# Performance work log

Measured on AMD Instinct MI355X. Metric: run time of the kernel, lower is better.

Reference implementation:

```python
import jax, jax.numpy as jnp
import numpy as np


def setup_inputs() -> dict:
    key = jax.random.key(0)
    ks = jax.random.split(key, 11)
    B, S, D = 2, 2048, 1024
    s = 0.02
    return {
        "query": jax.random.normal(ks[0], (B, S, D), jnp.float32),
        "key": jax.random.normal(ks[1], (B, S, D), jnp.float32),
        "value": jax.random.normal(ks[2], (B, S, D), jnp.float32),
        "Wq": jax.random.normal(ks[3], (D, D), jnp.float32) * s,
        "bq": jnp.zeros((D,), jnp.float32),
        "Wk": jax.random.normal(ks[4], (D, D), jnp.float32) * s,
        "bk": jnp.zeros((D,), jnp.float32),
        "Wv": jax.random.normal(ks[5], (D, D), jnp.float32) * s,
        "bv": jnp.zeros((D,), jnp.float32),
        "Wo": jax.random.normal(ks[6], (D, D), jnp.float32) * s,
        "bo": jnp.zeros((D,), jnp.float32),
        "nheads": 16,
    }


def reference(query, key, value, Wq, bq, Wk, bk, Wv, bv, Wo, bo, nheads):
    B, Sq, D = query.shape
    Sk = key.shape[1]
    hd = D // nheads  # head dim
    q = (query @ Wq.T + bq).reshape(B, Sq, nheads, hd)
    k = (key @ Wk.T + bk).reshape(B, Sk, nheads, hd)
    v = (value @ Wv.T + bv).reshape(B, Sk, nheads, hd)
    score = jnp.einsum("bqhd,bkhd->bhqk", q, k)
    # mask == 'triu': strictly-upper-triangular entries set to -inf (causal)
    causal = jnp.triu(jnp.ones((Sq, Sk), dtype=bool), k=1)
    score = jnp.where(causal, -jnp.inf, score)
    # NOTE: original scales by sqrt(score.shape[-1]) == sqrt(kv_len), not sqrt(head_dim)
    scale = np.float32(1.0 / np.sqrt(Sk))
    att = jax.nn.softmax(score * scale, axis=-1)
    ret = jnp.einsum("bhqk,bkhd->bqhd", att, v).reshape(B, Sq, D)
    out = ret @ Wo.T + bo  # dropout is identity in eval mode
    return (out, att)
```

## Files before the change

### kernel.cpp

```cpp
#include <hip/hip_runtime.h>
#include <cstdint>
#include <cstddef>
#include <type_traits>

typedef __attribute__((ext_vector_type(8))) __bf16 bf16x8;
typedef __attribute__((ext_vector_type(4))) __bf16 bf16x4;
typedef __attribute__((ext_vector_type(4))) float f32x4;
typedef __attribute__((ext_vector_type(4))) unsigned short u16x4;

__device__ __forceinline__ f32x4 mfma16(bf16x8 a, bf16x8 b, f32x4 c) {
  return __builtin_amdgcn_mfma_f32_16x16x32_bf16(a, b, c, 0, 0, 0);
}

__device__ __forceinline__ void load_lds16(const void* g, void* l) {
  auto gp = reinterpret_cast<const __attribute__((address_space(1))) uint32_t*>(
      reinterpret_cast<uintptr_t>(g));
  auto lp = reinterpret_cast<__attribute__((address_space(3))) uint32_t*>(
      static_cast<uint32_t>(reinterpret_cast<uintptr_t>(l)));
  __builtin_amdgcn_global_load_lds(gp, lp, 16, 0, 0);
}

static constexpr float SCALE = 0.022097086912079608f;

static constexpr size_t OFF_XQ = 0;
static constexpr size_t OFF_XK = 4194304;
static constexpr size_t OFF_XV = 8388608;
static constexpr size_t OFF_WQ = 12582912;
static constexpr size_t OFF_WK = 13631488;
static constexpr size_t OFF_WV = 14680064;
static constexpr size_t OFF_WO = 15728640;
static constexpr size_t OFF_QB = 16777216;
static constexpr size_t OFF_KB = 20971520;
static constexpr size_t OFF_VT = 25165824;
static constexpr size_t OFF_RT = 29360128;

__global__ __launch_bounds__(256) void convert_all(
    const float* __restrict__ q, const float* __restrict__ k,
    const float* __restrict__ v, const float* __restrict__ wq,
    const float* __restrict__ wk, const float* __restrict__ wv,
    const float* __restrict__ wo, __bf16* __restrict__ ws)
{
  const int total = 2097152;
  for (int i = blockIdx.x * blockDim.x + threadIdx.x; i < total;
       i += gridDim.x * blockDim.x) {
    const float* src; size_t dstoff; int rel;
    if (i < 1572864) {
      if (i < 524288)       { src = q;  dstoff = OFF_XQ; rel = i; }
      else if (i < 1048576) { src = k;  dstoff = OFF_XK; rel = i - 524288; }
      else                  { src = v;  dstoff = OFF_XV; rel = i - 1048576; }
    } else if (i < 1835008) {
      if (i < 1703936)      { src = wq; dstoff = OFF_WQ; rel = i - 1572864; }
      else                  { src = wk; dstoff = OFF_WK; rel = i - 1703936; }
    } else if (i < 1966080) { src = wv; dstoff = OFF_WV; rel = i - 1835008; }
    else                    { src = wo; dstoff = OFF_WO; rel = i - 1966080; }
    float4 f0 = reinterpret_cast<const float4*>(src)[(size_t)rel * 2];
    float4 f1 = reinterpret_cast<const float4*>(src)[(size_t)rel * 2 + 1];
    bf16x8 o;
    o[0] = (__bf16)f0.x; o[1] = (__bf16)f0.y; o[2] = (__bf16)f0.z; o[3] = (__bf16)f0.w;
    o[4] = (__bf16)f1.x; o[5] = (__bf16)f1.y; o[6] = (__bf16)f1.z; o[7] = (__bf16)f1.w;
    *reinterpret_cast<bf16x8*>(ws + dstoff + (size_t)rel * 8) = o;
  }
}

__device__ __forceinline__ void gemm_body(
    const __bf16* __restrict__ A, const __bf16* __restrict__ Bm,
    const float* __restrict__ bias, void* __restrict__ Cout,
    int M, int N, int K, int mode, int m0, int n0,
    __bf16* As, __bf16* Bs)
{
  const int t = threadIdx.x;
  const int lane = t & 63, r = lane & 15, g = lane >> 4;
  const int w = t >> 6, wm = w >> 1, wn = w & 1;
  const int srow = t >> 3, scol = (t & 7) * 8;

  const f32x4 fzero = {0.f, 0.f, 0.f, 0.f};
  f32x4 acc[4][4];
#pragma unroll
  for (int x = 0; x < 4; x++)
#pragma unroll
    for (int y = 0; y < 4; y++) acc[x][y] = fzero;

  auto stage = [&](int buf, int k0) {
#pragma unroll
    for (int i = 0; i < 4; i++) {
      load_lds16(A  + (size_t)(m0 + i * 32 + srow) * K + k0 + scol, &As[buf * 8192 + i * 2048 + t * 8]);
      load_lds16(Bm + (size_t)(n0 + i * 32 + srow) * K + k0 + scol, &Bs[buf * 8192 + i * 2048 + t * 8]);
    }
  };

  const int NT = K / 64;
  stage(0, 0);
  asm volatile("s_waitcnt vmcnt(0)" ::: "memory");
  __syncthreads();
  int cur = 0;
  for (int kt = 0; kt < NT; ++kt) {
    if (kt + 1 < NT) stage(cur ^ 1, (kt + 1) * 64);
    const __bf16* Ab = &As[cur * 8192];
    const __bf16* Bb = &Bs[cur * 8192];
#pragma unroll
    for (int kk = 0; kk < 2; kk++) {
      bf16x8 af[4], bfv[4];
#pragma unroll
      for (int x = 0; x < 4; x++)
        af[x] = *reinterpret_cast<const bf16x8*>(&Ab[(wm * 64 + x * 16 + r) * 64 + kk * 32 + g * 8]);
#pragma unroll
      for (int y = 0; y < 4; y++)
        bfv[y] = *reinterpret_cast<const bf16x8*>(&Bb[(wn * 64 + y * 16 + r) * 64 + kk * 32 + g * 8]);
#pragma unroll
      for (int x = 0; x < 4; x++)
#pragma unroll
        for (int y = 0; y < 4; y++)
          acc[x][y] = mfma16(af[x], bfv[y], acc[x][y]);
    }
    asm volatile("s_waitcnt vmcnt(0)" ::: "memory");
    __syncthreads();
    cur ^= 1;
  }

#pragma unroll
  for (int x = 0; x < 4; x++)
#pragma unroll
    for (int y = 0; y < 4; y++) {
#pragma unroll
      for (int j = 0; j < 4; j++) {
        int row = m0 + wm * 64 + x * 16 + g * 4 + j;
        int col = n0 + wn * 64 + y * 16 + r;
        float val = acc[x][y][j];
        if (mode == 0 || mode == 1) {
          val += bias[col];
          int b = row >> 11, s = row & 2047, h = col >> 6, d = col & 63;
          ((__bf16*)Cout)[(((size_t)(b * 16 + h) * 2048 + s) << 6) + d] = (__bf16)val;
        } else if (mode == 2) {
          val += bias[row];
          int h = row >> 6, d = row & 63, b = col >> 11, s = col & 2047;
          ((__bf16*)Cout)[(((size_t)(b * 16 + h) * 64 + d) << 11) + s] = (__bf16)val;
        } else {
          val += bias[col];
          __builtin_nontemporal_store(val, &((float*)Cout)[(size_t)row * N + col]);
        }
      }
    }
}

__global__ __launch_bounds__(256) void gemm_qkv(
    __bf16* __restrict__ ws, const float* __restrict__ bq,
    const float* __restrict__ bk, const float* __restrict__ bv)
{
  __shared__ __align__(16) __bf16 As[2 * 8192];
  __shared__ __align__(16) __bf16 Bs[2 * 8192];
  const int z = blockIdx.z;
  if (z == 0) {
    gemm_body(ws + OFF_XQ, ws + OFF_WQ, bq, ws + OFF_QB, 4096, 1024, 1024, 0,
              blockIdx.y * 128, blockIdx.x * 128, As, Bs);
  } else if (z == 1) {
    gemm_body(ws + OFF_XK, ws + OFF_WK, bk, ws + OFF_KB, 4096, 1024, 1024, 1,
              blockIdx.y * 128, blockIdx.x * 128, As, Bs);
  } else {
    gemm_body(ws + OFF_WV, ws + OFF_XV, bv, ws + OFF_VT, 1024, 4096, 1024, 2,
              blockIdx.x * 128, blockIdx.y * 128, As, Bs);
  }
}

__global__ __launch_bounds__(256) void gemm_o(
    const __bf16* __restrict__ Rt, const __bf16* __restrict__ Wo,
    const float* __restrict__ bo, float* __restrict__ out)
{
  __shared__ __align__(16) __bf16 As[2 * 8192];
  __shared__ __align__(16) __bf16 Bs[2 * 8192];
  gemm_body(Rt, Wo, bo, out, 4096, 1024, 1024, 3,
            blockIdx.y * 128, blockIdx.x * 128, As, Bs);
}

__global__ __launch_bounds__(256) void attn_kernel(
    const __bf16* __restrict__ Qb, const __bf16* __restrict__ Kb,
    const __bf16* __restrict__ Vt, __bf16* __restrict__ Rt,
    float* __restrict__ att)
{
  __shared__ __align__(16) __bf16 Ks[128 * 68];
  __shared__ __align__(16) __bf16 Vts[64 * 132];
  __shared__ __align__(16) __bf16 Ps[128 * 132];

  const int t = threadIdx.x;
  const int lane = t & 63, r = lane & 15, g = lane >> 4;
  const int w = t >> 6;
  const int p = blockIdx.x;
  const int workid = (p & 7) * 64 + (p >> 3);
  const int bh = workid >> 4;
  const int xx = workid & 15;
  const int qb = ((bh >> 1) & 1) ? 15 - xx : xx;
  const int q0 = qb * 128;
  const __bf16* Qg = Qb + (size_t)bh * 2048 * 64;
  const __bf16* Kg = Kb + (size_t)bh * 2048 * 64;
  const __bf16* Vg = Vt + (size_t)bh * 64 * 2048;
  float* attb = att + (size_t)bh * 2048 * 2048 + (size_t)q0 * 2048;

  const int lrow = t >> 3, lcol = (t & 7) * 8;
  const int vrow = t >> 4, vcol = (t & 15) * 8;

  const f32x4 fzero = {0.f, 0.f, 0.f, 0.f};

  bf16x8 aq[2][2];
#pragma unroll
  for (int mf = 0; mf < 2; mf++)
#pragma unroll
    for (int kk = 0; kk < 2; kk++)
      aq[mf][kk] = *reinterpret_cast<const bf16x8*>(
          Qg + (size_t)(q0 + w * 32 + mf * 16 + r) * 64 + kk * 32 + g * 8);

  auto compute_scores = [&](f32x4(&accs)[2][8]) {
#pragma unroll
    for (int mf = 0; mf < 2; mf++)
#pragma unroll
      for (int nf = 0; nf < 8; nf++) accs[mf][nf] = fzero;
    __builtin_amdgcn_s_setprio(1);
#pragma unroll
    for (int kk = 0; kk < 2; kk++) {
#pragma unroll
      for (int nf = 0; nf < 8; nf++) {
        bf16x8 bk = *reinterpret_cast<const bf16x8*>(&Ks[(nf * 16 + r) * 68 + kk * 32 + g * 8]);
        accs[0][nf] = mfma16(aq[0][kk], bk, accs[0][nf]);
        accs[1][nf] = mfma16(aq[1][kk], bk, accs[1][nf]);
      }
    }
    __builtin_amdgcn_s_setprio(0);
  };

  float rs[2][4];
#pragma unroll
  for (int mf = 0; mf < 2; mf++)
#pragma unroll
    for (int j = 0; j < 4; j++) rs[mf][j] = 0.f;

  bf16x8 rk[4];
#pragma unroll
  for (int i = 0; i < 4; i++)
    rk[i] = *reinterpret_cast<const bf16x8*>(Kg + (size_t)(i * 32 + lrow) * 64 + lcol);

  for (int kt = 0; kt <= qb; ++kt) {
    __syncthreads();
#pragma unroll
    for (int i = 0; i < 4; i++)
      *reinterpret_cast<bf16x8*>(&Ks[(i * 32 + lrow) * 68 + lcol]) = rk[i];
    __syncthreads();
    if (kt < qb) {
#pragma unroll
      for (int i = 0; i < 4; i++)
        rk[i] = *reinterpret_cast<const bf16x8*>(Kg + (size_t)((kt + 1) * 128 + i * 32 + lrow) * 64 + lcol);
    }
    f32x4 accs[2][8];
    compute_scores(accs);

    auto p1body = [&](auto maskc) {
      constexpr bool MASK = decltype(maskc)::value;
#pragma unroll
      for (int mf = 0; mf < 2; mf++) {
        float es[4] = {0.f, 0.f, 0.f, 0.f};
#pragma unroll
        for (int nf = 0; nf < 8; nf++) {
          int col = kt * 128 + nf * 16 + r;
#pragma unroll
          for (int j = 0; j < 4; j++) {
            float e = __expf(accs[mf][nf][j] * SCALE);
            if (MASK) {
              int rowg = q0 + w * 32 + mf * 16 + g * 4 + j;
              e = (col <= rowg) ? e : 0.f;
            }
            es[j] += e;
          }
        }
#pragma unroll
        for (int j = 0; j < 4; j++) {
          float v2 = es[j];
          v2 += __shfl_xor(v2, 1, 64);
          v2 += __shfl_xor(v2, 2, 64);
          v2 += __shfl_xor(v2, 4, 64);
          v2 += __shfl_xor(v2, 8, 64);
          rs[mf][j] += v2;
        }
      }
    };
    if (kt == qb) p1body(std::integral_constant<bool, true>{});
    else          p1body(std::integral_constant<bool, false>{});
  }

  float rl[2][4];
#pragma unroll
  for (int mf = 0; mf < 2; mf++)
#pragma unroll
    for (int j = 0; j < 4; j++) rl[mf][j] = 1.0f / rs[mf][j];

  f32x4 accr[2][4];
#pragma unroll
  for (int mf = 0; mf < 2; mf++)
#pragma unroll
    for (int nf = 0; nf < 4; nf++) accr[mf][nf] = fzero;

  bf16x8 rv[4];
#pragma unroll
  for (int i = 0; i < 4; i++) {
    rk[i] = *reinterpret_cast<const bf16x8*>(Kg + (size_t)(i * 32 + lrow) * 64 + lcol);
    rv[i] = *reinterpret_cast<const bf16x8*>(Vg + (size_t)(i * 16 + vrow) * 2048 + vcol);
  }

  for (int kt = 0; kt <= qb; ++kt) {
    __syncthreads();
#pragma unroll
    for (int i = 0; i < 4; i++) {
      *reinterpret_cast<bf16x8*>(&Ks[(i * 32 + lrow) * 68 + lcol]) = rk[i];
      *reinterpret_cast<bf16x8*>(&Vts[(i * 16 + vrow) * 132 + vcol]) = rv[i];
    }
    __syncthreads();
    if (kt < qb) {
#pragma unroll
      for (int i = 0; i < 4; i++) {
        rk[i] = *reinterpret_cast<const bf16x8*>(Kg + (size_t)((kt + 1) * 128 + i * 32 + lrow) * 64 + lcol);
        rv[i] = *reinterpret_cast<const bf16x8*>(Vg + (size_t)(i * 16 + vrow) * 2048 + (kt + 1) * 128 + vcol);
      }
    }
    f32x4 accs[2][8];
    compute_scores(accs);

    auto p2body = [&](auto maskc) {
      constexpr bool MASK = decltype(maskc)::value;
#pragma unroll
      for (int mf = 0; mf < 2; mf++) {
#pragma unroll
        for (int nf = 0; nf < 8; nf++) {
          int col = kt * 128 + nf * 16 + r;
#pragma unroll
          for (int j = 0; j < 4; j++) {
            int rowl = w * 32 + mf * 16 + g * 4 + j;
            float e = __expf(accs[mf][nf][j] * SCALE);
            if (MASK) {
              e = (col <= q0 + rowl) ? e : 0.f;
            }
            float pp = e * rl[mf][j];
            Ps[rowl * 132 + nf * 16 + r] = (__bf16)pp;
          }
        }
      }
    };
    if (kt == qb) p2body(std::integral_constant<bool, true>{});
    else          p2body(std::integral_constant<bool, false>{});

    __syncthreads();
    __builtin_amdgcn_s_setprio(1);
#pragma unroll
    for (int kk2 = 0; kk2 < 4; kk2++) {
      bf16x8 ap0 = *reinterpret_cast<const bf16x8*>(&Ps[(w * 32 + r) * 132 + kk2 * 32 + g * 8]);
      bf16x8 ap1 = *reinterpret_cast<const bf16x8*>(&Ps[(w * 32 + 16 + r) * 132 + kk2 * 32 + g * 8]);
#pragma unroll
      for (int nf2 = 0; nf2 < 4; nf2++) {
        bf16x8 bv_ = *reinterpret_cast<const bf16x8*>(&Vts[(nf2 * 16 + r) * 132 + kk2 * 32 + g * 8]);
        accr[0][nf2] = mfma16(ap0, bv_, accr[0][nf2]);
        accr[1][nf2] = mfma16(ap1, bv_, accr[1][nf2]);
      }
    }
    __builtin_amdgcn_s_setprio(0);

    {
      const int crow8 = t >> 5;
      const int c4 = t & 31;
#pragma unroll
      for (int j = 0; j < 16; j++) {
        int row = j * 8 + crow8;
        u16x4 pv = *reinterpret_cast<const u16x4*>(&Ps[row * 132 + c4 * 4]);
        f32x4 f;
        f[0] = __uint_as_float((unsigned)pv[0] << 16);
        f[1] = __uint_as_float((unsigned)pv[1] << 16);
        f[2] = __uint_as_float((unsigned)pv[2] << 16);
        f[3] = __uint_as_float((unsigned)pv[3] << 16);
        __builtin_nontemporal_store(
            f, reinterpret_cast<f32x4*>(attb + (size_t)row * 2048 + kt * 128 + c4 * 4));
      }
    }
  }

  const f32x4 z4 = {0.f, 0.f, 0.f, 0.f};
  for (int kt2 = qb + 1; kt2 < 16; ++kt2) {
    for (int idx = t; idx < 4096; idx += 256) {
      int row = idx >> 5, c4 = idx & 31;
      __builtin_nontemporal_store(
          z4, reinterpret_cast<f32x4*>(attb + (size_t)row * 2048 + kt2 * 128 + c4 * 4));
    }
  }

  const int b = bh >> 4, h = bh & 15;
#pragma unroll
  for (int mf = 0; mf < 2; mf++)
#pragma unroll
    for (int nf2 = 0; nf2 < 4; nf2++)
#pragma unroll
      for (int j = 0; j < 4; j++) {
        int qrow = q0 + w * 32 + mf * 16 + g * 4 + j;
        int d = nf2 * 16 + r;
        Rt[((size_t)(b * 2048 + qrow) << 10) + h * 64 + d] = (__bf16)accr[mf][nf2][j];
      }
}

extern "C" void kernel_launch(void* const* d_in, const int* in_sizes, int n_in,
                              void* d_out, int out_size, void* d_ws, size_t ws_size,
                              hipStream_t stream) {
  (void)in_sizes; (void)n_in; (void)out_size; (void)ws_size;
  const float* q  = (const float*)d_in[0];
  const float* k  = (const float*)d_in[1];
  const float* v  = (const float*)d_in[2];
  const float* wq = (const float*)d_in[3];
  const float* bq = (const float*)d_in[4];
  const float* wk = (const float*)d_in[5];
  const float* bk = (const float*)d_in[6];
  const float* wv = (const float*)d_in[7];
  const float* bv = (const float*)d_in[8];
  const float* wo = (const float*)d_in[9];
  const float* bo = (const float*)d_in[10];
  __bf16* ws = (__bf16*)d_ws;
  float* out = (float*)d_out;
  float* att = out + 4194304;

  convert_all<<<2048, 256, 0, stream>>>(q, k, v, wq, wk, wv, wo, ws);
  gemm_qkv<<<dim3(8, 32, 3), 256, 0, stream>>>(ws, bq, bk, bv);
  attn_kernel<<<512, 256, 0, stream>>>(ws + OFF_QB, ws + OFF_KB, ws + OFF_VT, ws + OFF_RT, att);
  gemm_o<<<dim3(8, 32), 256, 0, stream>>>(ws + OFF_RT, ws + OFF_WO, bo, out);
}
```

Before: 217.4 us.

## Keep attention probabilities in registers via transposed QK and double-buffered K/V

Computes S^T (K as the A operand) so each lane holds four consecutive key columns for one query row. This lets probabilities be written straight to the fp32 attention output and reused in registers as the PV MFMA A operand, with no LDS staging buffer. It double-buffers K/V in LDS to drop one barrier per tile, reduces row sums with two cross-lane shuffles, and uses exp2 with a prescaled constant. The attention output is now stored in full fp32 rather than bf16-rounded values. The direct per-lane 16-byte stores may coalesce worse than the old row-wise stores.

After: 294.2 us. 35.3% more time.

```diff
diff --git a/kernel.cpp b/kernel.cpp
--- a/kernel.cpp
+++ b/kernel.cpp
@@ -6,7 +6,6 @@
 typedef __attribute__((ext_vector_type(8))) __bf16 bf16x8;
 typedef __attribute__((ext_vector_type(4))) __bf16 bf16x4;
 typedef __attribute__((ext_vector_type(4))) float f32x4;
-typedef __attribute__((ext_vector_type(4))) unsigned short u16x4;
 
 __device__ __forceinline__ f32x4 mfma16(bf16x8 a, bf16x8 b, f32x4 c) {
   return __builtin_amdgcn_mfma_f32_16x16x32_bf16(a, b, c, 0, 0, 0);
@@ -20,7 +19,7 @@
   __builtin_amdgcn_global_load_lds(gp, lp, 16, 0, 0);
 }
 
-static constexpr float SCALE = 0.022097086912079608f;
+static constexpr float SC2 = 0.031879357f;
 
 static constexpr size_t OFF_XQ = 0;
 static constexpr size_t OFF_XK = 4194304;
@@ -176,9 +175,8 @@
     const __bf16* __restrict__ Vt, __bf16* __restrict__ Rt,
     float* __restrict__ att)
 {
-  __shared__ __align__(16) __bf16 Ks[128 * 68];
-  __shared__ __align__(16) __bf16 Vts[64 * 132];
-  __shared__ __align__(16) __bf16 Ps[128 * 132];
+  __shared__ __align__(16) __bf16 Kdb[2][128 * 68];
+  __shared__ __align__(16) __bf16 Vdb[2][64 * 132];
 
   const int t = threadIdx.x;
   const int lane = t & 63, r = lane & 15, g = lane >> 4;
@@ -201,179 +199,160 @@
 
   bf16x8 aq[2][2];
 #pragma unroll
-  for (int mf = 0; mf < 2; mf++)
+  for (int nf = 0; nf < 2; nf++)
 #pragma unroll
     for (int kk = 0; kk < 2; kk++)
-      aq[mf][kk] = *reinterpret_cast<const bf16x8*>(
-          Qg + (size_t)(q0 + w * 32 + mf * 16 + r) * 64 + kk * 32 + g * 8);
-
-  auto compute_scores = [&](f32x4(&accs)[2][8]) {
-#pragma unroll
-    for (int mf = 0; mf < 2; mf++)
-#pragma unroll
-      for (int nf = 0; nf < 8; nf++) accs[mf][nf] = fzero;
+      aq[nf][kk] = *reinterpret_cast<const bf16x8*>(
+          Qg + (size_t)(q0 + w * 32 + nf * 16 + r) * 64 + kk * 32 + g * 8);
+
+  const int myrow = q0 + w * 32 + r;
+
+  auto qk_scores = [&](const __bf16* Kl, f32x4(&accs)[8][2]) {
+#pragma unroll
+    for (int mf = 0; mf < 8; mf++) {
+      accs[mf][0] = fzero; accs[mf][1] = fzero;
+    }
     __builtin_amdgcn_s_setprio(1);
 #pragma unroll
     for (int kk = 0; kk < 2; kk++) {
 #pragma unroll
-      for (int nf = 0; nf < 8; nf++) {
-        bf16x8 bk = *reinterpret_cast<const bf16x8*>(&Ks[(nf * 16 + r) * 68 + kk * 32 + g * 8]);
-        accs[0][nf] = mfma16(aq[0][kk], bk, accs[0][nf]);
-        accs[1][nf] = mfma16(aq[1][kk], bk, accs[1][nf]);
+      for (int mf = 0; mf < 8; mf++) {
+        bf16x8 kf = *reinterpret_cast<const bf16x8*>(&Kl[(mf * 16 + r) * 68 + kk * 32 + g * 8]);
+        accs[mf][0] = mfma16(kf, aq[0][kk], accs[mf][0]);
+        accs[mf][1] = mfma16(kf, aq[1][kk], accs[mf][1]);
       }
     }
     __builtin_amdgcn_s_setprio(0);
   };
 
-  float rs[2][4];
-#pragma unroll
-  for (int mf = 0; mf < 2; mf++)
-#pragma unroll
-    for (int j = 0; j < 4; j++) rs[mf][j] = 0.f;
-
-  bf16x8 rk[4];
-#pragma unroll
-  for (int i = 0; i < 4; i++)
-    rk[i] = *reinterpret_cast<const bf16x8*>(Kg + (size_t)(i * 32 + lrow) * 64 + lcol);
+  bf16x8 rk[4], rv[4];
+  auto loadK = [&](int kt2) {
+#pragma unroll
+    for (int i = 0; i < 4; i++)
+      rk[i] = *reinterpret_cast<const bf16x8*>(Kg + (size_t)(kt2 * 128 + i * 32 + lrow) * 64 + lcol);
+  };
+  auto loadV = [&](int kt2) {
+#pragma unroll
+    for (int i = 0; i < 4; i++)
+      rv[i] = *reinterpret_cast<const bf16x8*>(Vg + (size_t)(i * 16 + vrow) * 2048 + kt2 * 128 + vcol);
+  };
+  auto writeK = [&](int buf) {
+#pragma unroll
+    for (int i = 0; i < 4; i++)
+      *reinterpret_cast<bf16x8*>(&Kdb[buf][(i * 32 + lrow) * 68 + lcol]) = rk[i];
+  };
+  auto writeV = [&](int buf) {
+#pragma unroll
+    for (int i = 0; i < 4; i++)
+      *reinterpret_cast<bf16x8*>(&Vdb[buf][(i * 16 + vrow) * 132 + vcol]) = rv[i];
+  };
+
+  loadK(0);
+  writeK(0);
+  if (qb > 0) loadK(1);
+  float part0 = 0.f, part1 = 0.f;
 
   for (int kt = 0; kt <= qb; ++kt) {
     __syncthreads();
-#pragma unroll
-    for (int i = 0; i < 4; i++)
-      *reinterpret_cast<bf16x8*>(&Ks[(i * 32 + lrow) * 68 + lcol]) = rk[i];
-    __syncthreads();
     if (kt < qb) {
-#pragma unroll
-      for (int i = 0; i < 4; i++)
-        rk[i] = *reinterpret_cast<const bf16x8*>(Kg + (size_t)((kt + 1) * 128 + i * 32 + lrow) * 64 + lcol);
-    }
-    f32x4 accs[2][8];
-    compute_scores(accs);
+      writeK((kt + 1) & 1);
+      if (kt + 2 <= qb) loadK(kt + 2);
+    }
+    f32x4 accs[8][2];
+    qk_scores(Kdb[kt & 1], accs);
 
     auto p1body = [&](auto maskc) {
       constexpr bool MASK = decltype(maskc)::value;
 #pragma unroll
-      for (int mf = 0; mf < 2; mf++) {
-        float es[4] = {0.f, 0.f, 0.f, 0.f};
-#pragma unroll
-        for (int nf = 0; nf < 8; nf++) {
-          int col = kt * 128 + nf * 16 + r;
+      for (int mf = 0; mf < 8; mf++)
+#pragma unroll
+        for (int nf = 0; nf < 2; nf++)
 #pragma unroll
           for (int j = 0; j < 4; j++) {
-            float e = __expf(accs[mf][nf][j] * SCALE);
+            float e = exp2f(accs[mf][nf][j] * SC2);
             if (MASK) {
-              int rowg = q0 + w * 32 + mf * 16 + g * 4 + j;
-              e = (col <= rowg) ? e : 0.f;
+              int kp = kt * 128 + mf * 16 + g * 4 + j;
+              e = (kp <= myrow + nf * 16) ? e : 0.f;
             }
-            es[j] += e;
+            if (nf) part1 += e; else part0 += e;
           }
-        }
-#pragma unroll
-        for (int j = 0; j < 4; j++) {
-          float v2 = es[j];
-          v2 += __shfl_xor(v2, 1, 64);
-          v2 += __shfl_xor(v2, 2, 64);
-          v2 += __shfl_xor(v2, 4, 64);
-          v2 += __shfl_xor(v2, 8, 64);
-          rs[mf][j] += v2;
-        }
-      }
     };
     if (kt == qb) p1body(std::integral_constant<bool, true>{});
     else          p1body(std::integral_constant<bool, false>{});
   }
-
-  float rl[2][4];
+  part0 += __shfl_xor(part0, 16, 64);
+  part0 += __shfl_xor(part0, 32, 64);
+  part1 += __shfl_xor(part1, 16, 64);
+  part1 += __shfl_xor(part1, 32, 64);
+  const float rl0 = 1.0f / part0, rl1 = 1.0f / part1;
+
+  f32x4 accr[2][4];
 #pragma unroll
   for (int mf = 0; mf < 2; mf++)
 #pragma unroll
-    for (int j = 0; j < 4; j++) rl[mf][j] = 1.0f / rs[mf][j];
-
-  f32x4 accr[2][4];
-#pragma unroll
-  for (int mf = 0; mf < 2; mf++)
-#pragma unroll
-    for (int nf = 0; nf < 4; nf++) accr[mf][nf] = fzero;
-
-  bf16x8 rv[4];
-#pragma unroll
-  for (int i = 0; i < 4; i++) {
-    rk[i] = *reinterpret_cast<const bf16x8*>(Kg + (size_t)(i * 32 + lrow) * 64 + lcol);
-    rv[i] = *reinterpret_cast<const bf16x8*>(Vg + (size_t)(i * 16 + vrow) * 2048 + vcol);
-  }
+    for (int nf2 = 0; nf2 < 4; nf2++) accr[mf][nf2] = fzero;
+
+  __syncthreads();
+  loadK(0); loadV(0);
+  writeK(0); writeV(0);
+  if (qb > 0) { loadK(1); loadV(1); }
+
+  float* attrow0 = attb + (size_t)(w * 32 + r) * 2048 + 4 * g;
 
   for (int kt = 0; kt <= qb; ++kt) {
     __syncthreads();
-#pragma unroll
-    for (int i = 0; i < 4; i++) {
-      *reinterpret_cast<bf16x8*>(&Ks[(i * 32 + lrow) * 68 + lcol]) = rk[i];
-      *reinterpret_cast<bf16x8*>(&Vts[(i * 16 + vrow) * 132 + vcol]) = rv[i];
-    }
-    __syncthreads();
     if (kt < qb) {
-#pragma unroll
-      for (int i = 0; i < 4; i++) {
-        rk[i] = *reinterpret_cast<const bf16x8*>(Kg + (size_t)((kt + 1) * 128 + i * 32 + lrow) * 64 + lcol);
-        rv[i] = *reinterpret_cast<const bf16x8*>(Vg + (size_t)(i * 16 + vrow) * 2048 + (kt + 1) * 128 + vcol);
-      }
-    }
-    f32x4 accs[2][8];
-    compute_scores(accs);
-
+      writeK((kt + 1) & 1); writeV((kt + 1) & 1);
+      if (kt + 2 <= qb) { loadK(kt + 2); loadV(kt + 2); }
+    }
+    f32x4 accs[8][2];
+    qk_scores(Kdb[kt & 1], accs);
+
+    bf16x4 pkv[2][8];
     auto p2body = [&](auto maskc) {
       constexpr bool MASK = decltype(maskc)::value;
 #pragma unroll
-      for (int mf = 0; mf < 2; mf++) {
-#pragma unroll
-        for (int nf = 0; nf < 8; nf++) {
-          int col = kt * 128 + nf * 16 + r;
+      for (int mf = 0; mf < 8; mf++)
+#pragma unroll
+        for (int nf = 0; nf < 2; nf++) {
+          f32x4 pv;
 #pragma unroll
           for (int j = 0; j < 4; j++) {
-            int rowl = w * 32 + mf * 16 + g * 4 + j;
-            float e = __expf(accs[mf][nf][j] * SCALE);
+            float e = exp2f(accs[mf][nf][j] * SC2);
             if (MASK) {
-              e = (col <= q0 + rowl) ? e : 0.f;
+              int kp = kt * 128 + mf * 16 + g * 4 + j;
+              e = (kp <= myrow + nf * 16) ? e : 0.f;
             }
-            float pp = e * rl[mf][j];
-            Ps[rowl * 132 + nf * 16 + r] = (__bf16)pp;
+            pv[j] = e * (nf ? rl1 : rl0);
           }
+          __builtin_nontemporal_store(
+              pv, reinterpret_cast<f32x4*>(attrow0 + (size_t)nf * 16 * 2048 + kt * 128 + mf * 16));
+          bf16x4 pb;
+          pb[0] = (__bf16)pv[0]; pb[1] = (__bf16)pv[1];
+          pb[2] = (__bf16)pv[2]; pb[3] = (__bf16)pv[3];
+          pkv[nf][mf] = pb;
         }
-      }
     };
     if (kt == qb) p2body(std::integral_constant<bool, true>{});
     else          p2body(std::integral_constant<bool, false>{});
 
-    __syncthreads();
+    const __bf16* Vl = Vdb[kt & 1];
     __builtin_amdgcn_s_setprio(1);
 #pragma unroll
     for (int kk2 = 0; kk2 < 4; kk2++) {
-      bf16x8 ap0 = *reinterpret_cast<const bf16x8*>(&Ps[(w * 32 + r) * 132 + kk2 * 32 + g * 8]);
-      bf16x8 ap1 = *reinterpret_cast<const bf16x8*>(&Ps[(w * 32 + 16 + r) * 132 + kk2 * 32 + g * 8]);
+      bf16x8 pa0 = __builtin_shufflevector(pkv[0][2 * kk2], pkv[0][2 * kk2 + 1], 0, 1, 2, 3, 4, 5, 6, 7);
+      bf16x8 pa1 = __builtin_shufflevector(pkv[1][2 * kk2], pkv[1][2 * kk2 + 1], 0, 1, 2, 3, 4, 5, 6, 7);
 #pragma unroll
       for (int nf2 = 0; nf2 < 4; nf2++) {
-        bf16x8 bv_ = *reinterpret_cast<const bf16x8*>(&Vts[(nf2 * 16 + r) * 132 + kk2 * 32 + g * 8]);
-        accr[0][nf2] = mfma16(ap0, bv_, accr[0][nf2]);
-        accr[1][nf2] = mfma16(ap1, bv_, accr[1][nf2]);
+        const __bf16* vb0 = &Vl[(nf2 * 16 + r) * 132 + kk2 * 32 + 4 * g];
+        bf16x4 x0 = *reinterpret_cast<const bf16x4*>(vb0);
+        bf16x4 x1 = *reinterpret_cast<const bf16x4*>(vb0 + 16);
+        bf16x8 vb = __builtin_shufflevector(x0, x1, 0, 1, 2, 3, 4, 5, 6, 7);
+        accr[0][nf2] = mfma16(pa0, vb, accr[0][nf2]);
+        accr[1][nf2] = mfma16(pa1, vb, accr[1][nf2]);
       }
     }
     __builtin_amdgcn_s_setprio(0);
-
-    {
-      const int crow8 = t >> 5;
-      const int c4 = t & 31;
-#pragma unroll
-      for (int j = 0; j < 16; j++) {
-        int row = j * 8 + crow8;
-        u16x4 pv = *reinterpret_cast<const u16x4*>(&Ps[row * 132 + c4 * 4]);
-        f32x4 f;
-        f[0] = __uint_as_float((unsigned)pv[0] << 16);
-        f[1] = __uint_as_float((unsigned)pv[1] << 16);
-        f[2] = __uint_as_float((unsigned)pv[2] << 16);
-        f[3] = __uint_as_float((unsigned)pv[3] << 16);
-        __builtin_nontemporal_store(
-            f, reinterpret_cast<f32x4*>(attb + (size_t)row * 2048 + kt * 128 + c4 * 4));
-      }
-    }
   }
 
   const f32x4 z4 = {0.f, 0.f, 0.f, 0.f};
```

## Double-buffer K tiles, cut barriers, defer row-sum reduction, use exp2

Applied to the files above, without the earlier changes.

Pass 1 now double-buffers K tiles in LDS, reusing the idle P buffer as the second slot, so each iteration needs one barrier instead of two. Pass 2 reorganizes the loop so each wave writes only its own P rows to the attention output, which removes the barrier between the P write and the PV MFMA. The next K/V tile is staged into LDS after the output stores, with the global loads issued two tiles ahead. Row-sum shuffles move out of the loop into a single reduction at the end, and __expf with a scale becomes exp2f with a log2e-prescaled constant. The buffer-aliasing scheme adds extra ordering constraints that have to hold for correctness.

Result: slower. 350.5 us (+61.2%).

```diff
diff --git a/kernel.cpp b/kernel.cpp
--- a/kernel.cpp
+++ b/kernel.cpp
@@ -20,7 +20,7 @@
   __builtin_amdgcn_global_load_lds(gp, lp, 16, 0, 0);
 }
 
-static constexpr float SCALE = 0.022097086912079608f;
+static constexpr float SC2 = 0.031879357f;
 
 static constexpr size_t OFF_XQ = 0;
 static constexpr size_t OFF_XK = 4194304;
@@ -176,9 +176,10 @@
     const __bf16* __restrict__ Vt, __bf16* __restrict__ Rt,
     float* __restrict__ att)
 {
-  __shared__ __align__(16) __bf16 Ks[128 * 68];
-  __shared__ __align__(16) __bf16 Vts[64 * 132];
-  __shared__ __align__(16) __bf16 Ps[128 * 132];
+  __shared__ __align__(16) __bf16 smem[34048];
+  __bf16* Ks  = smem;
+  __bf16* Vts = smem + 8704;
+  __bf16* Ps  = smem + 17152;
 
   const int t = threadIdx.x;
   const int lane = t & 63, r = lane & 15, g = lane >> 4;
@@ -207,7 +208,7 @@
       aq[mf][kk] = *reinterpret_cast<const bf16x8*>(
           Qg + (size_t)(q0 + w * 32 + mf * 16 + r) * 64 + kk * 32 + g * 8);
 
-  auto compute_scores = [&](f32x4(&accs)[2][8]) {
+  auto compute_scores = [&](const __bf16* Kl, f32x4(&accs)[2][8]) {
 #pragma unroll
     for (int mf = 0; mf < 2; mf++)
 #pragma unroll
@@ -217,7 +218,7 @@
     for (int kk = 0; kk < 2; kk++) {
 #pragma unroll
       for (int nf = 0; nf < 8; nf++) {
-        bf16x8 bk = *reinterpret_cast<const bf16x8*>(&Ks[(nf * 16 + r) * 68 + kk * 32 + g * 8]);
+        bf16x8 bk = *reinterpret_cast<const bf16x8*>(&Kl[(nf * 16 + r) * 68 + kk * 32 + g * 8]);
         accs[0][nf] = mfma16(aq[0][kk], bk, accs[0][nf]);
         accs[1][nf] = mfma16(aq[1][kk], bk, accs[1][nf]);
       }
@@ -225,59 +226,64 @@
     __builtin_amdgcn_s_setprio(0);
   };
 
-  float rs[2][4];
+  bf16x8 rk[4], rv[4];
+  auto loadK = [&](int kt2) {
+#pragma unroll
+    for (int i = 0; i < 4; i++)
+      rk[i] = *reinterpret_cast<const bf16x8*>(Kg + (size_t)(kt2 * 128 + i * 32 + lrow) * 64 + lcol);
+  };
+  auto loadV = [&](int kt2) {
+#pragma unroll
+    for (int i = 0; i < 4; i++)
+      rv[i] = *reinterpret_cast<const bf16x8*>(Vg + (size_t)(i * 16 + vrow) * 2048 + kt2 * 128 + vcol);
+  };
+  auto writeKto = [&](__bf16* dst) {
+#pragma unroll
+    for (int i = 0; i < 4; i++)
+      *reinterpret_cast<bf16x8*>(&dst[(i * 32 + lrow) * 68 + lcol]) = rk[i];
+  };
+  auto writeV = [&]() {
+#pragma unroll
+    for (int i = 0; i < 4; i++)
+      *reinterpret_cast<bf16x8*>(&Vts[(i * 16 + vrow) * 132 + vcol]) = rv[i];
+  };
+
+  float rsp[2][4];
 #pragma unroll
   for (int mf = 0; mf < 2; mf++)
 #pragma unroll
-    for (int j = 0; j < 4; j++) rs[mf][j] = 0.f;
-
-  bf16x8 rk[4];
-#pragma unroll
-  for (int i = 0; i < 4; i++)
-    rk[i] = *reinterpret_cast<const bf16x8*>(Kg + (size_t)(i * 32 + lrow) * 64 + lcol);
+    for (int j = 0; j < 4; j++) rsp[mf][j] = 0.f;
+
+  loadK(0);
+  writeKto(Ks);
+  if (qb > 0) loadK(1);
 
   for (int kt = 0; kt <= qb; ++kt) {
     __syncthreads();
-#pragma unroll
-    for (int i = 0; i < 4; i++)
-      *reinterpret_cast<bf16x8*>(&Ks[(i * 32 + lrow) * 68 + lcol]) = rk[i];
-    __syncthreads();
     if (kt < qb) {
-#pragma unroll
-      for (int i = 0; i < 4; i++)
-        rk[i] = *reinterpret_cast<const bf16x8*>(Kg + (size_t)((kt + 1) * 128 + i * 32 + lrow) * 64 + lcol);
+      writeKto(((kt + 1) & 1) ? Ps : Ks);
+      if (kt + 2 <= qb) loadK(kt + 2);
     }
     f32x4 accs[2][8];
-    compute_scores(accs);
+    compute_scores((kt & 1) ? Ps : Ks, accs);
 
     auto p1body = [&](auto maskc) {
       constexpr bool MASK = decltype(maskc)::value;
 #pragma unroll
-      for (int mf = 0; mf < 2; mf++) {
-        float es[4] = {0.f, 0.f, 0.f, 0.f};
+      for (int mf = 0; mf < 2; mf++)
 #pragma unroll
         for (int nf = 0; nf < 8; nf++) {
           int col = kt * 128 + nf * 16 + r;
 #pragma unroll
           for (int j = 0; j < 4; j++) {
-            float e = __expf(accs[mf][nf][j] * SCALE);
+            float e = exp2f(accs[mf][nf][j] * SC2);
             if (MASK) {
               int rowg = q0 + w * 32 + mf * 16 + g * 4 + j;
               e = (col <= rowg) ? e : 0.f;
             }
-            es[j] += e;
+            rsp[mf][j] += e;
           }
         }
-#pragma unroll
-        for (int j = 0; j < 4; j++) {
-          float v2 = es[j];
-          v2 += __shfl_xor(v2, 1, 64);
-          v2 += __shfl_xor(v2, 2, 64);
-          v2 += __shfl_xor(v2, 4, 64);
-          v2 += __shfl_xor(v2, 8, 64);
-          rs[mf][j] += v2;
-        }
-      }
     };
     if (kt == qb) p1body(std::integral_constant<bool, true>{});
     else          p1body(std::integral_constant<bool, false>{});
@@ -287,38 +293,30 @@
 #pragma unroll
   for (int mf = 0; mf < 2; mf++)
 #pragma unroll
-    for (int j = 0; j < 4; j++) rl[mf][j] = 1.0f / rs[mf][j];
+    for (int j = 0; j < 4; j++) {
+      float v2 = rsp[mf][j];
+      v2 += __shfl_xor(v2, 1, 64);
+      v2 += __shfl_xor(v2, 2, 64);
+      v2 += __shfl_xor(v2, 4, 64);
+      v2 += __shfl_xor(v2, 8, 64);
+      rl[mf][j] = 1.0f / v2;
+    }
 
   f32x4 accr[2][4];
 #pragma unroll
   for (int mf = 0; mf < 2; mf++)
 #pragma unroll
-    for (int nf = 0; nf < 4; nf++) accr[mf][nf] = fzero;
-
-  bf16x8 rv[4];
-#pragma unroll
-  for (int i = 0; i < 4; i++) {
-    rk[i] = *reinterpret_cast<const bf16x8*>(Kg + (size_t)(i * 32 + lrow) * 64 + lcol);
-    rv[i] = *reinterpret_cast<const bf16x8*>(Vg + (size_t)(i * 16 + vrow) * 2048 + vcol);
-  }
+    for (int nf2 = 0; nf2 < 4; nf2++) accr[mf][nf2] = fzero;
+
+  loadK(0); loadV(0);
+  __syncthreads();
+  writeKto(Ks); writeV();
+  if (qb > 0) { loadK(1); loadV(1); }
 
   for (int kt = 0; kt <= qb; ++kt) {
     __syncthreads();
-#pragma unroll
-    for (int i = 0; i < 4; i++) {
-      *reinterpret_cast<bf16x8*>(&Ks[(i * 32 + lrow) * 68 + lcol]) = rk[i];
-      *reinterpret_cast<bf16x8*>(&Vts[(i * 16 + vrow) * 132 + vcol]) = rv[i];
-    }
-    __syncthreads();
-    if (kt < qb) {
-#pragma unroll
-      for (int i = 0; i < 4; i++) {
-        rk[i] = *reinterpret_cast<const bf16x8*>(Kg + (size_t)((kt + 1) * 128 + i * 32 + lrow) * 64 + lcol);
-        rv[i] = *reinterpret_cast<const bf16x8*>(Vg + (size_t)(i * 16 + vrow) * 2048 + (kt + 1) * 128 + vcol);
-      }
-    }
     f32x4 accs[2][8];
-    compute_scores(accs);
+    compute_scores(Ks, accs);
 
     auto p2body = [&](auto maskc) {
       constexpr bool MASK = decltype(maskc)::value;
@@ -330,7 +328,7 @@
 #pragma unroll
           for (int j = 0; j < 4; j++) {
             int rowl = w * 32 + mf * 16 + g * 4 + j;
-            float e = __expf(accs[mf][nf][j] * SCALE);
+            float e = exp2f(accs[mf][nf][j] * SC2);
             if (MASK) {
               e = (col <= q0 + rowl) ? e : 0.f;
             }
@@ -343,7 +341,6 @@
     if (kt == qb) p2body(std::integral_constant<bool, true>{});
     else          p2body(std::integral_constant<bool, false>{});
 
-    __syncthreads();
     __builtin_amdgcn_s_setprio(1);
 #pragma unroll
     for (int kk2 = 0; kk2 < 4; kk2++) {
@@ -359,20 +356,26 @@
     __builtin_amdgcn_s_setprio(0);
 
     {
-      const int crow8 = t >> 5;
-      const int c4 = t & 31;
+      const int half = (lane >> 5);
+      const int c4 = lane & 31;
 #pragma unroll
       for (int j = 0; j < 16; j++) {
-        int row = j * 8 + crow8;
-        u16x4 pv = *reinterpret_cast<const u16x4*>(&Ps[row * 132 + c4 * 4]);
+        int rowl = w * 32 + 2 * j + half;
+        u16x4 pv = *reinterpret_cast<const u16x4*>(&Ps[rowl * 132 + c4 * 4]);
         f32x4 f;
         f[0] = __uint_as_float((unsigned)pv[0] << 16);
         f[1] = __uint_as_float((unsigned)pv[1] << 16);
         f[2] = __uint_as_float((unsigned)pv[2] << 16);
         f[3] = __uint_as_float((unsigned)pv[3] << 16);
         __builtin_nontemporal_store(
-            f, reinterpret_cast<f32x4*>(attb + (size_t)row * 2048 + kt * 128 + c4 * 4));
-      }
+            f, reinterpret_cast<f32x4*>(attb + (size_t)rowl * 2048 + kt * 128 + c4 * 4));
+      }
+    }
+
+    __syncthreads();
+    if (kt < qb) {
+      writeKto(Ks); writeV();
+      if (kt + 2 <= qb) { loadK(kt + 2); loadV(kt + 2); }
     }
   }
 
```
